# Kernel tuning notes

Hardware: AMD Instinct MI355X
Metric: run time of the kernel (lower is better)

Reference implementation:

```python
import jax, jax.numpy as jnp
import numpy as np

EMBED_DIM = 1024
NUM_HEADS = 16
HEAD_DIM = EMBED_DIM // NUM_HEADS
FF_HIDDEN = 4096
ROPE_BASE = 10000.0


def rope(x, start_pos):
    # x: [B, H, S, hd]; interleaved pair rotation
    S, hd = x.shape[2], x.shape[3]
    freqs = 1.0 / ROPE_BASE ** (jnp.arange(0, hd, 2, dtype=jnp.float32) / hd)
    t = jnp.arange(start_pos, start_pos + S, dtype=jnp.float32)
    angles = jnp.outer(t, freqs)            # [S, hd/2]
    cos, sin = jnp.cos(angles), jnp.sin(angles)
    x_even = x[..., 0::2]
    x_odd = x[..., 1::2]
    out_even = x_even * cos - x_odd * sin
    out_odd = x_even * sin + x_odd * cos
    return jnp.stack((out_even, out_odd), axis=-1).reshape(x.shape)


def rmsnorm(x, w, eps=1e-6):
    rms = jnp.sqrt(jnp.mean(x * x, axis=-1, keepdims=True) + eps)
    return x / rms * w


def setup_inputs() -> dict:
    key = jax.random.key(0)
    ks = jax.random.split(key, 8)
    D, H = EMBED_DIM, FF_HIDDEN
    s = lambda fin: 1.0 / np.sqrt(fin)
    return {
        "x": jax.random.normal(ks[0], (2, 2048, D), dtype=jnp.float32),
        "start_pos": 0,
        "norm1_w": jnp.ones((D,), jnp.float32),
        "w_qkv": jax.random.uniform(ks[1], (3 * D, D), jnp.float32, -s(D), s(D)),
        "w_o": jax.random.uniform(ks[2], (D, D), jnp.float32, -s(D), s(D)),
        "norm2_w": jnp.ones((D,), jnp.float32),
        "w_gate": jax.random.uniform(ks[3], (H, D), jnp.float32, -s(D), s(D)),
        "w_up": jax.random.uniform(ks[4], (H, D), jnp.float32, -s(D), s(D)),
        "w_down": jax.random.uniform(ks[5], (D, H), jnp.float32, -s(H), s(H)),
    }


def attention(x, w_qkv, w_o, start_pos):
    B, S, D = x.shape
    qkv = x @ w_qkv.T                         # [B, S, 3D]
    q, k, v = jnp.split(qkv, 3, axis=-1)
    def heads(t):
        return t.reshape(B, S, NUM_HEADS, HEAD_DIM).transpose(0, 2, 1, 3)
    q, k, v = heads(q), heads(k), heads(v)    # [B, H, S, hd]
    q = rope(q, start_pos)
    k = rope(k, start_pos)
    scores = jnp.einsum('bhqd,bhkd->bhqk', q, k) / np.sqrt(HEAD_DIM)
    causal = jnp.tril(jnp.ones((S, S), dtype=bool))
    scores = jnp.where(causal, scores, -jnp.inf)
    attn = jax.nn.softmax(scores, axis=-1)
    out = jnp.einsum('bhqk,bhkd->bhqd', attn, v)
    out = out.transpose(0, 2, 1, 3).reshape(B, S, D)
    return out @ w_o.T


def ffn(x, w_gate, w_up, w_down):
    return (jax.nn.silu(x @ w_gate.T) * (x @ w_up.T)) @ w_down.T


def reference(x, start_pos, norm1_w, w_qkv, w_o, norm2_w, w_gate, w_up, w_down):
    x = x + attention(rmsnorm(x, norm1_w), w_qkv, w_o, start_pos)
    x = x + ffn(rmsnorm(x, norm2_w), w_gate, w_up, w_down)
    return x
```

## Files before the change

### kernel.cpp

```cpp
#include <hip/hip_runtime.h>
#include <math.h>

typedef __bf16 bf16_t;
typedef __bf16 bf16x2 __attribute__((ext_vector_type(2)));
typedef __bf16 bf16x4 __attribute__((ext_vector_type(4)));
typedef __bf16 bf16x8 __attribute__((ext_vector_type(8)));
typedef float f32x4 __attribute__((ext_vector_type(4)));

#define B_ 2
#define S_ 2048
#define D_ 1024
#define NH 16
#define HD 64
#define FF 4096
#define NTOK (B_*S_)

__device__ __forceinline__ f32x4 mfma16(bf16x8 a, bf16x8 b, f32x4 c) {
  return __builtin_amdgcn_mfma_f32_16x16x32_bf16(a, b, c, 0, 0, 0);
}

__device__ __forceinline__ void gld_lds16(const bf16_t* g, bf16_t* l) {
  __builtin_amdgcn_global_load_lds(
      (const __attribute__((address_space(1))) void*)g,
      (__attribute__((address_space(3))) void*)l, 16, 0, 0);
}

__global__ __launch_bounds__(256) void cvt_kernel(const float* __restrict__ in,
                                                  bf16_t* __restrict__ o, int n4) {
  int i = blockIdx.x * 256 + threadIdx.x;
  const int stride = gridDim.x * 256;
  for (; i < n4; i += stride) {
    float4 v = ((const float4*)in)[i];
    bf16x4 ov;
    ov[0] = (bf16_t)v.x; ov[1] = (bf16_t)v.y; ov[2] = (bf16_t)v.z; ov[3] = (bf16_t)v.w;
    ((bf16x4*)o)[i] = ov;
  }
}

__global__ __launch_bounds__(256) void rmsnorm_kernel(const float* __restrict__ x,
                                                      const float* __restrict__ w,
                                                      bf16_t* __restrict__ o) {
  const int row = blockIdx.x;
  const float4 v = ((const float4*)(x + (size_t)row * D_))[threadIdx.x];
  float s = v.x*v.x + v.y*v.y + v.z*v.z + v.w*v.w;
  #pragma unroll
  for (int d = 32; d; d >>= 1) s += __shfl_down(s, d);
  __shared__ float acc[4];
  if ((threadIdx.x & 63) == 0) acc[threadIdx.x >> 6] = s;
  __syncthreads();
  const float scale = rsqrtf((acc[0] + acc[1] + acc[2] + acc[3]) * (1.f / D_) + 1e-6f);
  const float4 wv = ((const float4*)w)[threadIdx.x];
  bf16x4 ov;
  ov[0] = (bf16_t)(v.x * scale * wv.x);
  ov[1] = (bf16_t)(v.y * scale * wv.y);
  ov[2] = (bf16_t)(v.z * scale * wv.z);
  ov[3] = (bf16_t)(v.w * scale * wv.w);
  ((bf16x4*)(o + (size_t)row * D_))[threadIdx.x] = ov;
}

template<int MODE, int BN>
__global__ __launch_bounds__(256) void gemm_kernel(
    const bf16_t* __restrict__ A, const bf16_t* __restrict__ W,
    int M, int N, int K,
    float* __restrict__ outF, bf16_t* __restrict__ outB,
    const float* __restrict__ res, const bf16_t* __restrict__ gate) {
  constexpr int NB = BN / 32;
  __shared__ __align__(16) bf16_t lA[128 * 32];
  __shared__ __align__(16) bf16_t lB[BN * 32];
  const int tid = threadIdx.x;
  const int wave = tid >> 6, lane = tid & 63;
  const int r = lane & 15, kg = lane >> 4;
  const int bm = blockIdx.y * 128, bn = blockIdx.x * BN;
  const int wr = (wave >> 1) * 64, wc = (wave & 1) * (BN / 2);
  const bf16_t* Ab = A + (size_t)bm * K;
  const bf16_t* Wb = W + (size_t)bn * K;

  f32x4 acc[4][NB] = {};
  for (int k0 = 0; k0 < K; k0 += 32) {
    __syncthreads();
    {
      const int cb0 = (wave << 6);
      const int c0 = cb0 + lane;
      gld_lds16(Ab + (size_t)(c0 >> 2) * K + k0 + (c0 & 3) * 8, lA + cb0 * 8);
      const int cb1 = cb0 + 256;
      const int c1 = cb1 + lane;
      gld_lds16(Ab + (size_t)(c1 >> 2) * K + k0 + (c1 & 3) * 8, lA + cb1 * 8);
      if (BN == 128) {
        gld_lds16(Wb + (size_t)(c0 >> 2) * K + k0 + (c0 & 3) * 8, lB + cb0 * 8);
        gld_lds16(Wb + (size_t)(c1 >> 2) * K + k0 + (c1 & 3) * 8, lB + cb1 * 8);
      } else {
        gld_lds16(Wb + (size_t)(c0 >> 2) * K + k0 + (c0 & 3) * 8, lB + cb0 * 8);
      }
    }
    __syncthreads();
    bf16x8 af[4], bfr[NB];
    #pragma unroll
    for (int m = 0; m < 4; ++m)
      af[m] = *(const bf16x8*)&lA[(wr + m * 16 + r) * 32 + kg * 8];
    #pragma unroll
    for (int n = 0; n < NB; ++n)
      bfr[n] = *(const bf16x8*)&lB[(wc + n * 16 + r) * 32 + kg * 8];
    #pragma unroll
    for (int m = 0; m < 4; ++m)
      #pragma unroll
      for (int n = 0; n < NB; ++n)
        acc[m][n] = mfma16(af[m], bfr[n], acc[m][n]);
  }
  #pragma unroll
  for (int m = 0; m < 4; ++m) {
    const int row0 = bm + wr + m * 16 + kg * 4;
    #pragma unroll
    for (int n = 0; n < NB; ++n) {
      const int col = bn + wc + n * 16 + r;
      #pragma unroll
      for (int g2 = 0; g2 < 4; ++g2) {
        const size_t idx = (size_t)(row0 + g2) * N + col;
        const float v = acc[m][n][g2];
        if (MODE == 0) {
          outB[idx] = (bf16_t)v;
        } else if (MODE == 1) {
          outF[idx] = v + res[idx];
        } else {
          const float gf = (float)gate[idx];
          outB[idx] = (bf16_t)(v * gf / (1.f + __expf(-gf)));
        }
      }
    }
  }
}

__global__ __launch_bounds__(256) void rope_kernel(const bf16_t* __restrict__ qkv,
                                                   bf16_t* __restrict__ q_r,
                                                   bf16_t* __restrict__ k_r,
                                                   const int* __restrict__ start_pos) {
  const int bs = blockIdx.x;
  const int b = bs >> 11, s = bs & (S_ - 1);
  const float t = (float)(s + start_pos[0]);
  const bf16_t* rowp = qkv + (size_t)bs * 3072;
  #pragma unroll
  for (int i = 0; i < 4; ++i) {
    const int p = threadIdx.x + 256 * i;
    const int mat = p >> 9;
    const int rem = p & 511;
    const int h = rem >> 5, d2 = rem & 31;
    const float freq = exp2f((float)d2 * -0.4152410118609203f);
    float sn, cs;
    sincosf(t * freq, &sn, &cs);
    const bf16x2 e2 = *(const bf16x2*)(rowp + mat * 1024 + h * 64 + 2 * d2);
    const float e = (float)e2[0], od = (float)e2[1];
    bf16x2 ov;
    ov[0] = (bf16_t)(e * cs - od * sn);
    ov[1] = (bf16_t)(e * sn + od * cs);
    bf16_t* dst = (mat ? k_r : q_r) + ((size_t)(b * NH + h) * S_ + s) * HD + 2 * d2;
    *(bf16x2*)dst = ov;
  }
}

__global__ __launch_bounds__(256) void vtrans_kernel(const bf16_t* __restrict__ qkv,
                                                     bf16_t* __restrict__ vt) {
  const int bh = blockIdx.y, b = bh >> 4, h = bh & 15;
  const int s0 = blockIdx.x * 64;
  __shared__ bf16_t tile[64][65];
  #pragma unroll
  for (int i = 0; i < 16; ++i) {
    const int idx = threadIdx.x + 256 * i;
    const int sl = idx >> 6, d = idx & 63;
    tile[sl][d] = qkv[(size_t)(b * S_ + s0 + sl) * 3072 + 2048 + h * 64 + d];
  }
  __syncthreads();
  #pragma unroll
  for (int i = 0; i < 16; ++i) {
    const int idx = threadIdx.x + 256 * i;
    const int dl = idx >> 6, sl = idx & 63;
    vt[((size_t)bh * HD + dl) * S_ + s0 + sl] = tile[sl][dl];
  }
}

__global__ __launch_bounds__(256, 4) void attn_kernel(const bf16_t* __restrict__ qr,
                                                      const bf16_t* __restrict__ kr,
                                                      const bf16_t* __restrict__ vt,
                                                      bf16_t* __restrict__ out) {
  const int bh = blockIdx.y, b = bh >> 4, h = bh & 15;
  const int wave = threadIdx.x >> 6, lane = threadIdx.x & 63;
  const int pl = wave >> 1, sub = wave & 1;
  const int r = lane & 15, kg = lane >> 4;
  const int pairIdx = blockIdx.x * 2 + pl;
  const bf16_t* kb_p = kr + (size_t)bh * S_ * HD;
  const bf16_t* vb_p = vt + (size_t)bh * HD * S_;

  __shared__ __align__(16) f32x4 lo[2][4][64];
  __shared__ float lm[2][64], ll[2][64];

  auto run_chunk = [&](int qbase, f32x4* o, float& m, float& l) {
    const bf16_t* qp = qr + ((size_t)bh * S_ + qbase) * HD;
    const bf16x8 qf0 = *(const bf16x8*)&qp[r * HD + kg * 8];
    const bf16x8 qf1 = *(const bf16x8*)&qp[r * HD + 32 + kg * 8];
    const int limit = qbase + 16;
    for (int kb = sub * 64; kb < limit; kb += 128) {
      f32x4 st[4];
      #pragma unroll
      for (int f = 0; f < 4; ++f) {
        const bf16_t* kp = kb_p + (size_t)(kb + f * 16 + r) * HD;
        f32x4 z = {};
        z = mfma16(*(const bf16x8*)&kp[kg * 8], qf0, z);
        z = mfma16(*(const bf16x8*)&kp[32 + kg * 8], qf1, z);
        st[f] = z;
      }
      float sc[4][4];
      float mx = -1e30f;
      #pragma unroll
      for (int f = 0; f < 4; ++f)
        #pragma unroll
        for (int g2 = 0; g2 < 4; ++g2) {
          const int k = kb + f * 16 + kg * 4 + g2;
          const float v = (k <= qbase + r) ? st[f][g2] * 0.125f : -1e30f;
          sc[f][g2] = v;
          mx = fmaxf(mx, v);
        }
      mx = fmaxf(mx, __shfl_xor(mx, 16));
      mx = fmaxf(mx, __shfl_xor(mx, 32));
      const float nm = fmaxf(m, mx);
      const float alpha = __expf(m - nm);
      m = nm;
      float psum = 0.f;
      float pe[4][4];
      #pragma unroll
      for (int f = 0; f < 4; ++f)
        #pragma unroll
        for (int g2 = 0; g2 < 4; ++g2) {
          const float p = __expf(sc[f][g2] - nm);
          pe[f][g2] = p;
          psum += p;
        }
      psum += __shfl_xor(psum, 16);
      psum += __shfl_xor(psum, 32);
      l = l * alpha + psum;
      bf16x8 PA[2];
      #pragma unroll
      for (int fa = 0; fa < 2; ++fa) {
        bf16x8 v;
        #pragma unroll
        for (int j = 0; j < 4; ++j) v[j] = (bf16_t)pe[2 * fa][j];
        #pragma unroll
        for (int j = 0; j < 4; ++j) v[4 + j] = (bf16_t)pe[2 * fa + 1][j];
        PA[fa] = v;
      }
      float av[4];
      #pragma unroll
      for (int g2 = 0; g2 < 4; ++g2) av[g2] = __shfl(alpha, kg * 4 + g2);
      #pragma unroll
      for (int dblk = 0; dblk < 4; ++dblk)
        #pragma unroll
        for (int g2 = 0; g2 < 4; ++g2) o[dblk][g2] *= av[g2];
      #pragma unroll
      for (int dblk = 0; dblk < 4; ++dblk) {
        const bf16_t* vp = vb_p + (size_t)(dblk * 16 + r) * S_ + kb;
        #pragma unroll
        for (int fa = 0; fa < 2; ++fa) {
          union { bf16x8 v; bf16x4 hf[2]; } bv;
          bv.hf[0] = *(const bf16x4*)&vp[fa * 32 + kg * 4];
          bv.hf[1] = *(const bf16x4*)&vp[fa * 32 + 16 + kg * 4];
          o[dblk] = mfma16(PA[fa], bv.v, o[dblk]);
        }
      }
    }
  };

  auto write_partial = [&](const f32x4* o, float m, float l) {
    #pragma unroll
    for (int dblk = 0; dblk < 4; ++dblk) lo[pl][dblk][lane] = o[dblk];
    lm[pl][lane] = m;
    ll[pl][lane] = l;
  };

  auto finalize = [&](int qbase, const f32x4* o, float m, float l) {
    const float m1 = lm[pl][lane], l1 = ll[pl][lane];
    const float ms = fmaxf(m, m1);
    const float a0 = __expf(m - ms), a1 = __expf(m1 - ms);
    const float lt = l * a0 + l1 * a1;
    float av0[4], av1[4], lv[4];
    #pragma unroll
    for (int g2 = 0; g2 < 4; ++g2) {
      av0[g2] = __shfl(a0, kg * 4 + g2);
      av1[g2] = __shfl(a1, kg * 4 + g2);
      lv[g2]  = __shfl(lt, kg * 4 + g2);
    }
    #pragma unroll
    for (int dblk = 0; dblk < 4; ++dblk) {
      const f32x4 o1 = lo[pl][dblk][lane];
      #pragma unroll
      for (int g2 = 0; g2 < 4; ++g2) {
        const int srow = qbase + kg * 4 + g2;
        out[(size_t)(b * S_ + srow) * D_ + h * HD + dblk * 16 + r] =
            (bf16_t)((o[dblk][g2] * av0[g2] + o1[g2] * av1[g2]) / lv[g2]);
      }
    }
  };

  {
    const int qbase = pairIdx * 16;
    f32x4 o[4] = {};
    float m = -1e30f, l = 0.f;
    run_chunk(qbase, o, m, l);
    if (sub == 1) write_partial(o, m, l);
    __syncthreads();
    if (sub == 0) finalize(qbase, o, m, l);
  }
  {
    const int qbase = (127 - pairIdx) * 16;
    f32x4 o[4] = {};
    float m = -1e30f, l = 0.f;
    run_chunk(qbase, o, m, l);
    if (sub == 0) write_partial(o, m, l);
    __syncthreads();
    if (sub == 1) finalize(qbase, o, m, l);
  }
}

extern "C" void kernel_launch(void* const* d_in, const int* in_sizes, int n_in,
                              void* d_out, int out_size, void* d_ws, size_t ws_size,
                              hipStream_t stream) {
  const float* x     = (const float*)d_in[0];
  const int*   sp    = (const int*)d_in[1];
  const float* n1w   = (const float*)d_in[2];
  const float* wqkv  = (const float*)d_in[3];
  const float* wo    = (const float*)d_in[4];
  const float* n2w   = (const float*)d_in[5];
  const float* wgate = (const float*)d_in[6];
  const float* wup   = (const float*)d_in[7];
  const float* wdown = (const float*)d_in[8];

  char* p = (char*)d_ws;
  bf16_t* wqkv_b = (bf16_t*)p; p += (size_t)3 * D_ * D_ * 2;
  bf16_t* wo_b   = (bf16_t*)p; p += (size_t)D_ * D_ * 2;
  bf16_t* wg_b   = (bf16_t*)p; p += (size_t)FF * D_ * 2;
  bf16_t* wu_b   = (bf16_t*)p; p += (size_t)FF * D_ * 2;
  bf16_t* wd_b   = (bf16_t*)p; p += (size_t)FF * D_ * 2;
  bf16_t* xn     = (bf16_t*)p; p += (size_t)NTOK * D_ * 2;
  float*  x1     = (float*)p;  p += (size_t)NTOK * D_ * 4;
  char* pool = p;
  bf16_t* qkv    = (bf16_t*)(pool);
  bf16_t* q_r    = (bf16_t*)(pool + (size_t)25165824);
  bf16_t* k_r    = (bf16_t*)(pool + (size_t)33554432);
  bf16_t* v_t    = (bf16_t*)(pool + (size_t)41943040);
  bf16_t* attn_o = (bf16_t*)(pool + (size_t)50331648);
  bf16_t* gbuf   = (bf16_t*)(pool);
  bf16_t* hbuf   = (bf16_t*)(pool + (size_t)33554432);

  cvt_kernel<<<dim3(1024), dim3(256), 0, stream>>>(wqkv,  wqkv_b, 3 * D_ * D_ / 4);
  cvt_kernel<<<dim3(1024), dim3(256), 0, stream>>>(wo,    wo_b,   D_ * D_ / 4);
  cvt_kernel<<<dim3(1024), dim3(256), 0, stream>>>(wgate, wg_b,   FF * D_ / 4);
  cvt_kernel<<<dim3(1024), dim3(256), 0, stream>>>(wup,   wu_b,   FF * D_ / 4);
  cvt_kernel<<<dim3(1024), dim3(256), 0, stream>>>(wdown, wd_b,   FF * D_ / 4);

  rmsnorm_kernel<<<dim3(NTOK), dim3(256), 0, stream>>>(x, n1w, xn);

  gemm_kernel<0,128><<<dim3(3 * D_ / 128, NTOK / 128), dim3(256), 0, stream>>>(
      xn, wqkv_b, NTOK, 3 * D_, D_, nullptr, qkv, nullptr, nullptr);

  rope_kernel<<<dim3(NTOK), dim3(256), 0, stream>>>(qkv, q_r, k_r, sp);
  vtrans_kernel<<<dim3(S_ / 64, B_ * NH), dim3(256), 0, stream>>>(qkv, v_t);

  attn_kernel<<<dim3(32, B_ * NH), dim3(256), 0, stream>>>(q_r, k_r, v_t, attn_o);

  gemm_kernel<1,64><<<dim3(D_ / 64, NTOK / 128), dim3(256), 0, stream>>>(
      attn_o, wo_b, NTOK, D_, D_, x1, nullptr, x, nullptr);

  rmsnorm_kernel<<<dim3(NTOK), dim3(256), 0, stream>>>(x1, n2w, xn);

  gemm_kernel<0,128><<<dim3(FF / 128, NTOK / 128), dim3(256), 0, stream>>>(
      xn, wg_b, NTOK, FF, D_, nullptr, gbuf, nullptr, nullptr);

  gemm_kernel<2,128><<<dim3(FF / 128, NTOK / 128), dim3(256), 0, stream>>>(
      xn, wu_b, NTOK, FF, D_, nullptr, hbuf, nullptr, gbuf);

  gemm_kernel<1,64><<<dim3(D_ / 64, NTOK / 128), dim3(256), 0, stream>>>(
      hbuf, wd_b, NTOK, D_, FF, (float*)d_out, nullptr, x1, nullptr);
}
```

Measured before the change: 593.9 us.

## Double-buffer GEMM LDS, fuse weight casts, fold softmax scale into Q, remap attention blocks

The GEMM now uses two LDS buffers and issues the next K-slice's global-to-LDS loads before computing on the current one, so load latency overlaps with MFMA work. The five weight-cast launches are merged into one kernel. RoPE pre-scales Q by log2(e)/sqrt(d), which lets attention use exp2f without a per-score multiply. Attention also splits unmasked key blocks from the diagonal block, skips rescaling the output when the running max grows by no more than 8, and remaps block indices so the blocks of one head land on the same XCD for L2 locality. The extra LDS buffer and larger attention code may lower occupancy.

```diff
diff --git a/kernel.cpp b/kernel.cpp
--- a/kernel.cpp
+++ b/kernel.cpp
@@ -25,15 +25,35 @@
       (__attribute__((address_space(3))) void*)l, 16, 0, 0);
 }
 
-__global__ __launch_bounds__(256) void cvt_kernel(const float* __restrict__ in,
-                                                  bf16_t* __restrict__ o, int n4) {
+__global__ __launch_bounds__(256) void cvt5_kernel(
+    const float* __restrict__ p0, const float* __restrict__ p1,
+    const float* __restrict__ p2, const float* __restrict__ p3,
+    const float* __restrict__ p4,
+    bf16_t* __restrict__ o0, bf16_t* __restrict__ o1, bf16_t* __restrict__ o2,
+    bf16_t* __restrict__ o3, bf16_t* __restrict__ o4) {
   int i = blockIdx.x * 256 + threadIdx.x;
   const int stride = gridDim.x * 256;
-  for (; i < n4; i += stride) {
-    float4 v = ((const float4*)in)[i];
+  const int n = 4194304;
+  for (; i < n; i += stride) {
+    const float* src; bf16_t* dst; int j = i;
+    if (j < 786432) { src = p0; dst = o0; }
+    else {
+      j -= 786432;
+      if (j < 262144) { src = p1; dst = o1; }
+      else {
+        j -= 262144;
+        if (j < 1048576) { src = p2; dst = o2; }
+        else {
+          j -= 1048576;
+          if (j < 1048576) { src = p3; dst = o3; }
+          else { j -= 1048576; src = p4; dst = o4; }
+        }
+      }
+    }
+    float4 v = ((const float4*)src)[j];
     bf16x4 ov;
     ov[0] = (bf16_t)v.x; ov[1] = (bf16_t)v.y; ov[2] = (bf16_t)v.z; ov[3] = (bf16_t)v.w;
-    ((bf16x4*)o)[i] = ov;
+    ((bf16x4*)dst)[j] = ov;
   }
 }
 
@@ -65,8 +85,8 @@
     float* __restrict__ outF, bf16_t* __restrict__ outB,
     const float* __restrict__ res, const bf16_t* __restrict__ gate) {
   constexpr int NB = BN / 32;
-  __shared__ __align__(16) bf16_t lA[128 * 32];
-  __shared__ __align__(16) bf16_t lB[BN * 32];
+  __shared__ __align__(16) bf16_t lA[2][128 * 32];
+  __shared__ __align__(16) bf16_t lB[2][BN * 32];
   const int tid = threadIdx.x;
   const int wave = tid >> 6, lane = tid & 63;
   const int r = lane & 15, kg = lane >> 4;
@@ -75,36 +95,42 @@
   const bf16_t* Ab = A + (size_t)bm * K;
   const bf16_t* Wb = W + (size_t)bn * K;
 
+  auto stage = [&](int buf, int k0) {
+    const int cb0 = (wave << 6);
+    const int c0 = cb0 + lane;
+    gld_lds16(Ab + (size_t)(c0 >> 2) * K + k0 + (c0 & 3) * 8, lA[buf] + cb0 * 8);
+    const int cb1 = cb0 + 256;
+    const int c1 = cb1 + lane;
+    gld_lds16(Ab + (size_t)(c1 >> 2) * K + k0 + (c1 & 3) * 8, lA[buf] + cb1 * 8);
+    gld_lds16(Wb + (size_t)(c0 >> 2) * K + k0 + (c0 & 3) * 8, lB[buf] + cb0 * 8);
+    if (BN == 128)
+      gld_lds16(Wb + (size_t)(c1 >> 2) * K + k0 + (c1 & 3) * 8, lB[buf] + cb1 * 8);
+  };
+
   f32x4 acc[4][NB] = {};
+  stage(0, 0);
+  asm volatile("s_waitcnt vmcnt(0)" ::: "memory");
+  __syncthreads();
+  int cur = 0;
   for (int k0 = 0; k0 < K; k0 += 32) {
-    __syncthreads();
-    {
-      const int cb0 = (wave << 6);
-      const int c0 = cb0 + lane;
-      gld_lds16(Ab + (size_t)(c0 >> 2) * K + k0 + (c0 & 3) * 8, lA + cb0 * 8);
-      const int cb1 = cb0 + 256;
-      const int c1 = cb1 + lane;
-      gld_lds16(Ab + (size_t)(c1 >> 2) * K + k0 + (c1 & 3) * 8, lA + cb1 * 8);
-      if (BN == 128) {
-        gld_lds16(Wb + (size_t)(c0 >> 2) * K + k0 + (c0 & 3) * 8, lB + cb0 * 8);
-        gld_lds16(Wb + (size_t)(c1 >> 2) * K + k0 + (c1 & 3) * 8, lB + cb1 * 8);
-      } else {
-        gld_lds16(Wb + (size_t)(c0 >> 2) * K + k0 + (c0 & 3) * 8, lB + cb0 * 8);
-      }
-    }
-    __syncthreads();
+    if (k0 + 32 < K) stage(cur ^ 1, k0 + 32);
+    const bf16_t* cA = lA[cur];
+    const bf16_t* cB = lB[cur];
     bf16x8 af[4], bfr[NB];
     #pragma unroll
     for (int m = 0; m < 4; ++m)
-      af[m] = *(const bf16x8*)&lA[(wr + m * 16 + r) * 32 + kg * 8];
+      af[m] = *(const bf16x8*)&cA[(wr + m * 16 + r) * 32 + kg * 8];
     #pragma unroll
     for (int n = 0; n < NB; ++n)
-      bfr[n] = *(const bf16x8*)&lB[(wc + n * 16 + r) * 32 + kg * 8];
+      bfr[n] = *(const bf16x8*)&cB[(wc + n * 16 + r) * 32 + kg * 8];
     #pragma unroll
     for (int m = 0; m < 4; ++m)
       #pragma unroll
       for (int n = 0; n < NB; ++n)
         acc[m][n] = mfma16(af[m], bfr[n], acc[m][n]);
+    asm volatile("s_waitcnt vmcnt(0)" ::: "memory");
+    __syncthreads();
+    cur ^= 1;
   }
   #pragma unroll
   for (int m = 0; m < 4; ++m) {
@@ -146,11 +172,12 @@
     const float freq = exp2f((float)d2 * -0.4152410118609203f);
     float sn, cs;
     sincosf(t * freq, &sn, &cs);
+    const float qs = mat ? 1.0f : 0.18033688011112042f;
     const bf16x2 e2 = *(const bf16x2*)(rowp + mat * 1024 + h * 64 + 2 * d2);
     const float e = (float)e2[0], od = (float)e2[1];
     bf16x2 ov;
-    ov[0] = (bf16_t)(e * cs - od * sn);
-    ov[1] = (bf16_t)(e * sn + od * cs);
+    ov[0] = (bf16_t)((e * cs - od * sn) * qs);
+    ov[1] = (bf16_t)((e * sn + od * cs) * qs);
     bf16_t* dst = (mat ? k_r : q_r) + ((size_t)(b * NH + h) * S_ + s) * HD + 2 * d2;
     *(bf16x2*)dst = ov;
   }
@@ -180,90 +207,109 @@
                                                       const bf16_t* __restrict__ kr,
                                                       const bf16_t* __restrict__ vt,
                                                       bf16_t* __restrict__ out) {
-  const int bh = blockIdx.y, b = bh >> 4, h = bh & 15;
+  const int lid = blockIdx.x + 32 * blockIdx.y;
+  const int xcd = lid & 7, slot = lid >> 3;
+  const int bh = xcd * 4 + (slot >> 5);
+  const int bx = slot & 31;
+  const int b = bh >> 4, h = bh & 15;
   const int wave = threadIdx.x >> 6, lane = threadIdx.x & 63;
   const int pl = wave >> 1, sub = wave & 1;
   const int r = lane & 15, kg = lane >> 4;
-  const int pairIdx = blockIdx.x * 2 + pl;
+  const int pairIdx = bx * 2 + pl;
   const bf16_t* kb_p = kr + (size_t)bh * S_ * HD;
   const bf16_t* vb_p = vt + (size_t)bh * HD * S_;
 
   __shared__ __align__(16) f32x4 lo[2][4][64];
   __shared__ float lm[2][64], ll[2][64];
+
+  auto kv_block = [&](int kb, int qbase, const bf16x8& qf0, const bf16x8& qf1,
+                      f32x4* o, float& m, float& l, bool masked) {
+    f32x4 st[4];
+    #pragma unroll
+    for (int f = 0; f < 4; ++f) {
+      const bf16_t* kp = kb_p + (size_t)(kb + f * 16 + r) * HD;
+      f32x4 z = {};
+      z = mfma16(*(const bf16x8*)&kp[kg * 8], qf0, z);
+      z = mfma16(*(const bf16x8*)&kp[32 + kg * 8], qf1, z);
+      st[f] = z;
+    }
+    float sc[4][4];
+    float mx = -1e30f;
+    #pragma unroll
+    for (int f = 0; f < 4; ++f)
+      #pragma unroll
+      for (int g2 = 0; g2 < 4; ++g2) {
+        float v = st[f][g2];
+        if (masked) {
+          const int k = kb + f * 16 + kg * 4 + g2;
+          v = (k <= qbase + r) ? v : -1e30f;
+        }
+        sc[f][g2] = v;
+        mx = fmaxf(mx, v);
+      }
+    mx = fmaxf(mx, __shfl_xor(mx, 16));
+    mx = fmaxf(mx, __shfl_xor(mx, 32));
+    float alpha = 1.f;
+    const bool need = !__all(mx - m <= 8.f);
+    if (need) {
+      const float nm = fmaxf(m, mx);
+      alpha = exp2f(m - nm);
+      m = nm;
+    }
+    float psum = 0.f;
+    float pe[4][4];
+    #pragma unroll
+    for (int f = 0; f < 4; ++f)
+      #pragma unroll
+      for (int g2 = 0; g2 < 4; ++g2) {
+        const float p = exp2f(sc[f][g2] - m);
+        pe[f][g2] = p;
+        psum += p;
+      }
+    psum += __shfl_xor(psum, 16);
+    psum += __shfl_xor(psum, 32);
+    l = l * alpha + psum;
+    bf16x8 PA[2];
+    #pragma unroll
+    for (int fa = 0; fa < 2; ++fa) {
+      bf16x8 v;
+      #pragma unroll
+      for (int j = 0; j < 4; ++j) v[j] = (bf16_t)pe[2 * fa][j];
+      #pragma unroll
+      for (int j = 0; j < 4; ++j) v[4 + j] = (bf16_t)pe[2 * fa + 1][j];
+      PA[fa] = v;
+    }
+    if (need) {
+      float av[4];
+      #pragma unroll
+      for (int g2 = 0; g2 < 4; ++g2) av[g2] = __shfl(alpha, kg * 4 + g2);
+      #pragma unroll
+      for (int dblk = 0; dblk < 4; ++dblk)
+        #pragma unroll
+        for (int g2 = 0; g2 < 4; ++g2) o[dblk][g2] *= av[g2];
+    }
+    #pragma unroll
+    for (int dblk = 0; dblk < 4; ++dblk) {
+      const bf16_t* vp = vb_p + (size_t)(dblk * 16 + r) * S_ + kb;
+      #pragma unroll
+      for (int fa = 0; fa < 2; ++fa) {
+        union { bf16x8 v; bf16x4 hf[2]; } bv;
+        bv.hf[0] = *(const bf16x4*)&vp[fa * 32 + kg * 4];
+        bv.hf[1] = *(const bf16x4*)&vp[fa * 32 + 16 + kg * 4];
+        o[dblk] = mfma16(PA[fa], bv.v, o[dblk]);
+      }
+    }
+  };
 
   auto run_chunk = [&](int qbase, f32x4* o, float& m, float& l) {
     const bf16_t* qp = qr + ((size_t)bh * S_ + qbase) * HD;
     const bf16x8 qf0 = *(const bf16x8*)&qp[r * HD + kg * 8];
     const bf16x8 qf1 = *(const bf16x8*)&qp[r * HD + 32 + kg * 8];
-    const int limit = qbase + 16;
-    for (int kb = sub * 64; kb < limit; kb += 128) {
-      f32x4 st[4];
-      #pragma unroll
-      for (int f = 0; f < 4; ++f) {
-        const bf16_t* kp = kb_p + (size_t)(kb + f * 16 + r) * HD;
-        f32x4 z = {};
-        z = mfma16(*(const bf16x8*)&kp[kg * 8], qf0, z);
-        z = mfma16(*(const bf16x8*)&kp[32 + kg * 8], qf1, z);
-        st[f] = z;
-      }
-      float sc[4][4];
-      float mx = -1e30f;
-      #pragma unroll
-      for (int f = 0; f < 4; ++f)
-        #pragma unroll
-        for (int g2 = 0; g2 < 4; ++g2) {
-          const int k = kb + f * 16 + kg * 4 + g2;
-          const float v = (k <= qbase + r) ? st[f][g2] * 0.125f : -1e30f;
-          sc[f][g2] = v;
-          mx = fmaxf(mx, v);
-        }
-      mx = fmaxf(mx, __shfl_xor(mx, 16));
-      mx = fmaxf(mx, __shfl_xor(mx, 32));
-      const float nm = fmaxf(m, mx);
-      const float alpha = __expf(m - nm);
-      m = nm;
-      float psum = 0.f;
-      float pe[4][4];
-      #pragma unroll
-      for (int f = 0; f < 4; ++f)
-        #pragma unroll
-        for (int g2 = 0; g2 < 4; ++g2) {
-          const float p = __expf(sc[f][g2] - nm);
-          pe[f][g2] = p;
-          psum += p;
-        }
-      psum += __shfl_xor(psum, 16);
-      psum += __shfl_xor(psum, 32);
-      l = l * alpha + psum;
-      bf16x8 PA[2];
-      #pragma unroll
-      for (int fa = 0; fa < 2; ++fa) {
-        bf16x8 v;
-        #pragma unroll
-        for (int j = 0; j < 4; ++j) v[j] = (bf16_t)pe[2 * fa][j];
-        #pragma unroll
-        for (int j = 0; j < 4; ++j) v[4 + j] = (bf16_t)pe[2 * fa + 1][j];
-        PA[fa] = v;
-      }
-      float av[4];
-      #pragma unroll
-      for (int g2 = 0; g2 < 4; ++g2) av[g2] = __shfl(alpha, kg * 4 + g2);
-      #pragma unroll
-      for (int dblk = 0; dblk < 4; ++dblk)
-        #pragma unroll
-        for (int g2 = 0; g2 < 4; ++g2) o[dblk][g2] *= av[g2];
-      #pragma unroll
-      for (int dblk = 0; dblk < 4; ++dblk) {
-        const bf16_t* vp = vb_p + (size_t)(dblk * 16 + r) * S_ + kb;
-        #pragma unroll
-        for (int fa = 0; fa < 2; ++fa) {
-          union { bf16x8 v; bf16x4 hf[2]; } bv;
-          bv.hf[0] = *(const bf16x4*)&vp[fa * 32 + kg * 4];
-          bv.hf[1] = *(const bf16x4*)&vp[fa * 32 + 16 + kg * 4];
-          o[dblk] = mfma16(PA[fa], bv.v, o[dblk]);
-        }
-      }
-    }
+    int kb = sub * 64;
+    for (; kb + 64 <= qbase; kb += 128)
+      kv_block(kb, qbase, qf0, qf1, o, m, l, false);
+    if (kb < qbase + 16)
+      kv_block(kb, qbase, qf0, qf1, o, m, l, true);
   };
 
   auto write_partial = [&](const f32x4* o, float m, float l) {
@@ -276,7 +322,7 @@
   auto finalize = [&](int qbase, const f32x4* o, float m, float l) {
     const float m1 = lm[pl][lane], l1 = ll[pl][lane];
     const float ms = fmaxf(m, m1);
-    const float a0 = __expf(m - ms), a1 = __expf(m1 - ms);
+    const float a0 = exp2f(m - ms), a1 = exp2f(m1 - ms);
     const float lt = l * a0 + l1 * a1;
     float av0[4], av1[4], lv[4];
     #pragma unroll
@@ -347,11 +393,8 @@
   bf16_t* gbuf   = (bf16_t*)(pool);
   bf16_t* hbuf   = (bf16_t*)(pool + (size_t)33554432);
 
-  cvt_kernel<<<dim3(1024), dim3(256), 0, stream>>>(wqkv,  wqkv_b, 3 * D_ * D_ / 4);
-  cvt_kernel<<<dim3(1024), dim3(256), 0, stream>>>(wo,    wo_b,   D_ * D_ / 4);
-  cvt_kernel<<<dim3(1024), dim3(256), 0, stream>>>(wgate, wg_b,   FF * D_ / 4);
-  cvt_kernel<<<dim3(1024), dim3(256), 0, stream>>>(wup,   wu_b,   FF * D_ / 4);
-  cvt_kernel<<<dim3(1024), dim3(256), 0, stream>>>(wdown, wd_b,   FF * D_ / 4);
+  cvt5_kernel<<<dim3(2048), dim3(256), 0, stream>>>(
+      wqkv, wo, wgate, wup, wdown, wqkv_b, wo_b, wg_b, wu_b, wd_b);
 
   rmsnorm_kernel<<<dim3(NTOK), dim3(256), 0, stream>>>(x, n1w, xn);
 
```

Result: faster. 556.3 us (-6.3%).
